# Kernel optimization log

Hardware: AMD Instinct MI355X
Metric: run time of the kernel (lower is better)

Reference implementation:

```python
import jax, jax.numpy as jnp
import numpy as np

GAMMA = 1.0  # gamma=1, train_gamma=False -> constant
K = 3        # kernel_size


def _l2norm(x, axis=-1):
    return x / jnp.sqrt(jnp.sum(x * x, axis=axis, keepdims=True))


def setup_inputs() -> dict:
    key = jax.random.key(0)
    ks = jax.random.split(key, 9)
    B_img, R, D = 48, 36, 1024
    B_cap, T = 48, 32
    Dq = D // 4  # reduce_proj = 4
    s = lambda fan: 1.0 / np.sqrt(fan)
    return {
        "img_embed": jax.random.normal(ks[0], (B_img, R, D), jnp.float32),
        "cap_embed": jax.random.normal(ks[1], (B_cap, T, D), jnp.float32),
        "lens": jax.random.randint(ks[2], (B_cap,), 1, T),
        "Wred": jax.random.normal(ks[3], (Dq, D), jnp.float32) * s(D),
        "bred": jax.random.normal(ks[4], (Dq,), jnp.float32) * s(D),
        "Wproj": jax.random.normal(ks[5], (D * K, Dq), jnp.float32) * s(Dq),
        "bproj": jax.random.normal(ks[6], (D * K,), jnp.float32) * s(Dq),
        "Wconv": jax.random.normal(ks[7], (D, D), jnp.float32) * s(D),
        "bconv": jax.random.normal(ks[8], (D,), jnp.float32) * s(D),
    }


def reference(img_embed, cap_embed, lens, Wred, bred, Wproj, bproj, Wconv, bconv):
    # img_embed: (B, R, D) -> x: (B, D, R);  cap_embed: (Q, T, D)
    B, R, D = img_embed.shape
    Q = cap_embed.shape[0]
    x = jnp.transpose(img_embed, (0, 2, 1))  # (B, D, R)

    # red_txt Conv1d(D, D/4, 1): only token 0 is used downstream
    cap0 = cap_embed[:, 0, :]                                 # (Q, D)
    cap_repr = cap0 @ Wred.T + bred                           # (Q, D/4)

    # dynamic depthwise kernel, softmax-normalized over the K taps
    wdyn = (cap_repr @ Wproj.T + bproj).reshape(Q, D, K)      # (Q, D, K)
    wdyn = jax.nn.softmax(wdyn, axis=-1)

    # depthwise conv (padding=1) applied to the FULL image batch per caption
    xpad = jnp.pad(x, ((0, 0), (0, 0), (1, 1)))
    shifts = jnp.stack([xpad[:, :, h:h + R] for h in range(K)], axis=-1)  # (B,D,R,K)
    conv_dyn = jnp.einsum('bcrk,qck->qbcr', shifts, wdyn)      # (Q, B, D, R)

    # pointwise Conv1d(D, D, 1)
    y = jnp.einsum('qbcr,dc->qbdr', conv_dyn, Wconv) + bconv[None, None, :, None]

    # softmax gate over regions, gated sum-pool, l2norm, cosine sim
    mask = jax.nn.softmax(y * GAMMA, axis=-1)
    img_vec = _l2norm(jnp.sum(mask * y, axis=-1), axis=-1)     # (Q, B, D)
    cap_vec = _l2norm(cap0, axis=-1)                           # (Q, D)
    sims = jnp.einsum('qbd,qd->bq', img_vec, cap_vec)          # (B_img, B_cap)
    return sims
```

## Files before the change

### kernel.cpp

```cpp
#include <hip/hip_runtime.h>

#define D_   1024
#define B_   48
#define Q_   48
#define R_   36
#define RP_  38
#define DQ_  256
#define NPQ_ 1728

typedef __attribute__((ext_vector_type(8))) short bf16x8;
typedef __attribute__((ext_vector_type(8))) unsigned short u16x8;
typedef __attribute__((ext_vector_type(4))) float f32x4;

static __device__ __forceinline__ unsigned short f2bf(float f) {
  union { float f; unsigned u; } v; v.f = f;
  unsigned r = v.u + 0x7fffu + ((v.u >> 16) & 1u);
  return (unsigned short)(r >> 16);
}
static __device__ __forceinline__ float bf2f(unsigned short h) {
  union { unsigned u; float f; } v; v.u = ((unsigned)h) << 16; return v.f;
}
static __device__ __forceinline__ void gload_lds16(const void* g, void* s) {
  __builtin_amdgcn_global_load_lds(
      (const __attribute__((address_space(1))) unsigned int*)g,
      (__attribute__((address_space(3))) unsigned int*)s, 16, 0, 0);
}

__global__ __launch_bounds__(256) void k_capv(const float* __restrict__ cap_embed,
                                              float* __restrict__ capvec)
{
  const int q = blockIdx.x, t = threadIdx.x;
  const int w = t >> 6, lane = t & 63;
  __shared__ float red[4];
  float4 v = ((const float4*)(cap_embed + (size_t)q * 32 * D_))[t];
  float ss = v.x*v.x + v.y*v.y + v.z*v.z + v.w*v.w;
  #pragma unroll
  for (int off = 32; off > 0; off >>= 1) ss += __shfl_down(ss, off);
  if (lane == 0) red[w] = ss;
  __syncthreads();
  float rinv = rsqrtf(red[0] + red[1] + red[2] + red[3]);
  float4 cv; cv.x = v.x*rinv; cv.y = v.y*rinv; cv.z = v.z*rinv; cv.w = v.w*rinv;
  ((float4*)(capvec + (size_t)q * D_))[t] = cv;
}

__global__ __launch_bounds__(256) void k_repr(const float* __restrict__ cap_embed,
    const float* __restrict__ Wred, const float* __restrict__ bred,
    float* __restrict__ repr)
{
  const int q = blockIdx.x;
  const int w = threadIdx.x >> 6, lane = threadIdx.x & 63;
  const int o = blockIdx.y * 4 + w;
  const float4* c4 = (const float4*)(cap_embed + (size_t)q * 32 * D_);
  const float4* wr = (const float4*)(Wred + (size_t)o * D_);
  float acc = 0.f;
  #pragma unroll
  for (int j = 0; j < 4; j++) {
    float4 a = wr[lane + j*64], c = c4[lane + j*64];
    acc += a.x*c.x + a.y*c.y + a.z*c.z + a.w*c.w;
  }
  #pragma unroll
  for (int off = 32; off > 0; off >>= 1) acc += __shfl_down(acc, off);
  if (lane == 0) repr[(size_t)q * DQ_ + o] = acc + bred[o];
}

__global__ __launch_bounds__(256) void k_wdyn(const float* __restrict__ repr,
    const float* __restrict__ Wproj, const float* __restrict__ bproj,
    float* __restrict__ wpl)
{
  const int q = blockIdx.x;
  const int w = threadIdx.x >> 6, lane = threadIdx.x & 63;
  const int d = blockIdx.y * 4 + w;
  float4 r4 = ((const float4*)(repr + (size_t)q * DQ_))[lane];
  float a0, a1, a2;
  {
    const float4* p0 = (const float4*)(Wproj + (size_t)(d*3 + 0) * DQ_);
    const float4* p1 = (const float4*)(Wproj + (size_t)(d*3 + 1) * DQ_);
    const float4* p2 = (const float4*)(Wproj + (size_t)(d*3 + 2) * DQ_);
    float4 v0 = p0[lane], v1 = p1[lane], v2 = p2[lane];
    a0 = v0.x*r4.x + v0.y*r4.y + v0.z*r4.z + v0.w*r4.w;
    a1 = v1.x*r4.x + v1.y*r4.y + v1.z*r4.z + v1.w*r4.w;
    a2 = v2.x*r4.x + v2.y*r4.y + v2.z*r4.z + v2.w*r4.w;
  }
  #pragma unroll
  for (int off = 32; off > 0; off >>= 1) {
    a0 += __shfl_down(a0, off);
    a1 += __shfl_down(a1, off);
    a2 += __shfl_down(a2, off);
  }
  if (lane == 0) {
    float l0 = a0 + bproj[d*3], l1 = a1 + bproj[d*3+1], l2 = a2 + bproj[d*3+2];
    float m = fmaxf(l0, fmaxf(l1, l2));
    float e0 = __expf(l0-m), e1 = __expf(l1-m), e2 = __expf(l2-m);
    float inv = 1.0f / (e0 + e1 + e2);
    wpl[((size_t)q*3 + 0) * D_ + d] = e0 * inv;
    wpl[((size_t)q*3 + 1) * D_ + d] = e1 * inv;
    wpl[((size_t)q*3 + 2) * D_ + d] = e2 * inv;
  }
}

__global__ __launch_bounds__(256) void k_xpad(const float* __restrict__ img,
                                              unsigned short* __restrict__ xpb)
{
  const int br = blockIdx.x;
  const int b = br / RP_, rp = br % RP_;
  const int c = threadIdx.x * 4;
  short4 o;
  if (rp == 0 || rp == RP_ - 1) { o.x = 0; o.y = 0; o.z = 0; o.w = 0; }
  else {
    float4 v = *(const float4*)&img[((size_t)b * R_ + (rp-1)) * D_ + c];
    o.x = (short)f2bf(v.x); o.y = (short)f2bf(v.y);
    o.z = (short)f2bf(v.z); o.w = (short)f2bf(v.w);
  }
  *(short4*)&xpb[(size_t)br * D_ + c] = o;
}

__global__ __launch_bounds__(256) void k_wcbf(const float* __restrict__ Wconv,
                                              unsigned short* __restrict__ wcbf)
{
  const int tid = blockIdx.x * 256 + threadIdx.x;
  const int m = tid >> 7;
  const int gg = tid & 127;
  const int tile = gg >> 2, g = gg & 3;
  const int gl = g ^ ((m >> 1) & 3);
  const float* src = Wconv + (size_t)m * D_ + tile * 32 + gl * 8;
  float4 v0 = *(const float4*)src, v1 = *(const float4*)(src + 4);
  u16x8 o;
  o[0] = f2bf(v0.x); o[1] = f2bf(v0.y); o[2] = f2bf(v0.z); o[3] = f2bf(v0.w);
  o[4] = f2bf(v1.x); o[5] = f2bf(v1.y); o[6] = f2bf(v1.z); o[7] = f2bf(v1.w);
  *(u16x8*)&wcbf[(size_t)m * D_ + tile * 32 + g * 8] = o;
}

__global__ __launch_bounds__(256) void k_cd(const unsigned short* __restrict__ xpb,
    const float* __restrict__ wpl, unsigned short* __restrict__ cd, int qstart)
{
  const int ql = blockIdx.y, qg = qstart + ql;
  const int t = threadIdx.x;
  const int bloc = t >> 7;
  const int b = blockIdx.x * 2 + bloc;
  const int gg = t & 127;
  const int tile = gg >> 2, g = gg & 3;
  const int ch = gg * 8;

  float w0[8], w1[8], w2[8];
  {
    const float4* p0 = (const float4*)(wpl + ((size_t)qg*3 + 0)*D_ + ch);
    const float4* p1 = (const float4*)(wpl + ((size_t)qg*3 + 1)*D_ + ch);
    const float4* p2 = (const float4*)(wpl + ((size_t)qg*3 + 2)*D_ + ch);
    float4 a0 = p0[0], a1 = p0[1], b0 = p1[0], b1 = p1[1], d0 = p2[0], d1 = p2[1];
    w0[0]=a0.x; w0[1]=a0.y; w0[2]=a0.z; w0[3]=a0.w; w0[4]=a1.x; w0[5]=a1.y; w0[6]=a1.z; w0[7]=a1.w;
    w1[0]=b0.x; w1[1]=b0.y; w1[2]=b0.z; w1[3]=b0.w; w1[4]=b1.x; w1[5]=b1.y; w1[6]=b1.z; w1[7]=b1.w;
    w2[0]=d0.x; w2[1]=d0.y; w2[2]=d0.z; w2[3]=d0.w; w2[4]=d1.x; w2[5]=d1.y; w2[6]=d1.z; w2[7]=d1.w;
  }
  const unsigned short* xb = xpb + (size_t)b * RP_ * D_ + ch;
  u16x8 ra = *(const u16x8*)&xb[0];
  u16x8 rb = *(const u16x8*)&xb[D_];
  unsigned short* outb = cd + ((size_t)ql * NPQ_ + (size_t)b * R_) * D_ + tile * 32;
  for (int r = 0; r < R_; r++) {
    u16x8 rc = *(const u16x8*)&xb[(size_t)(r + 2) * D_];
    u16x8 o;
    #pragma unroll
    for (int i = 0; i < 8; i++) {
      float y = w0[i]*bf2f(ra[i]) + w1[i]*bf2f(rb[i]) + w2[i]*bf2f(rc[i]);
      o[i] = f2bf(y);
    }
    int gp = g ^ (((b * 36 + r) >> 1) & 3);
    *(u16x8*)&outb[(size_t)r * D_ + gp * 8] = o;
    ra = rb; rb = rc;
  }
}

#define BM_ 128
#define BN_ 144
#define BK_ 64

__global__ __launch_bounds__(256, 2) void k_gemm(
    const unsigned short* __restrict__ wcbf, const unsigned short* __restrict__ cd,
    const float* __restrict__ bconv, float* __restrict__ imgvec, int qstart)
{
  __shared__ __align__(16) unsigned char smem[37376];
  unsigned short* As = (unsigned short*)smem;
  unsigned short* Bs = (unsigned short*)(smem + 16384);
  float* ep = (float*)smem;

  const int t = threadIdx.x;
  const int w = t >> 6, lane = t & 63;
  const int nt0 = blockIdx.x * BN_;
  const int dt0 = blockIdx.y * BM_;
  const int ql = blockIdx.z, qg = qstart + ql;

  f32x4 acc[2][9];
  #pragma unroll
  for (int mm = 0; mm < 2; mm++)
    #pragma unroll
    for (int nt = 0; nt < 9; nt++)
      acc[mm][nt] = (f32x4){0.f, 0.f, 0.f, 0.f};

  const int lrow = lane >> 2;
  const int lc8  = (lane & 3) * 8;
  const unsigned short* Ag = wcbf + (size_t)dt0 * D_ + lc8;
  const unsigned short* Bg = cd + ((size_t)ql * NPQ_ + nt0) * D_ + lc8;
  const int fr = lane & 15;
  const int fro = fr * 32 + ((((lane >> 4) ^ ((fr >> 1) & 3))) << 3);

  for (int k0 = 0; k0 < D_; k0 += BK_) {
    #pragma unroll
    for (int jj = 0; jj < 2; jj++) {
      int j = w + jj * 4;
      #pragma unroll
      for (int h = 0; h < 2; h++)
        gload_lds16(Ag + (size_t)(j*16 + lrow) * D_ + k0 + h*32,
                    As + (j*2 + h) * 512);
    }
    for (int u = w; u < 18; u += 4) {
      int jb = u >> 1, h = u & 1;
      gload_lds16(Bg + (size_t)(jb*16 + lrow) * D_ + k0 + h*32,
                  Bs + u * 512);
    }
    __syncthreads();
    #pragma unroll
    for (int s = 0; s < 2; s++) {
      bf16x8 aF[2], bF[9];
      #pragma unroll
      for (int mm = 0; mm < 2; mm++)
        aF[mm] = *(const bf16x8*)&As[(w*4 + mm*2 + s) * 512 + fro];
      #pragma unroll
      for (int nt = 0; nt < 9; nt++)
        bF[nt] = *(const bf16x8*)&Bs[(nt*2 + s) * 512 + fro];
      #pragma unroll
      for (int mm = 0; mm < 2; mm++)
        #pragma unroll
        for (int nt = 0; nt < 9; nt++)
          acc[mm][nt] = __builtin_amdgcn_mfma_f32_16x16x32_bf16(aF[mm], bF[nt], acc[mm][nt], 0, 0, 0);
    }
    __syncthreads();
  }

  const int quad = lane >> 4;
  const int b0 = nt0 / R_;
  #pragma unroll
  for (int p = 0; p < 2; p++) {
    #pragma unroll
    for (int mm = 0; mm < 2; mm++)
      #pragma unroll
      for (int nt = 0; nt < 9; nt++) {
        int col = nt * 16 + fr;
        int cl = col - 72 * p;
        if (cl >= 0 && cl < 72) {
          #pragma unroll
          for (int rg = 0; rg < 4; rg++) {
            int row = w * 32 + mm * 16 + quad * 4 + rg;
            ep[row * 73 + cl] = acc[mm][nt][rg];
          }
        }
      }
    __syncthreads();
    {
      int dloc = t >> 1, bloc = t & 1;
      int bg = b0 + p * 2 + bloc;
      const float* yr = ep + dloc * 73 + bloc * 36;
      float m = yr[0];
      for (int r = 1; r < R_; r++) m = fmaxf(m, yr[r]);
      float s = 0.f, wsum = 0.f;
      for (int r = 0; r < R_; r++) {
        float yv = yr[r];
        float e = __expf(yv - m);
        s += e; wsum += e * yv;
      }
      float img = wsum / s + bconv[dt0 + dloc];
      imgvec[((size_t)qg * B_ + bg) * D_ + dt0 + dloc] = img;
    }
    __syncthreads();
  }
}

__global__ __launch_bounds__(256) void k_sims(const float* __restrict__ imgvec,
    const float* __restrict__ capvec, float* __restrict__ out)
{
  const int q = blockIdx.x, b = blockIdx.y, t = threadIdx.x;
  const float4* iv = (const float4*)(imgvec + ((size_t)q * B_ + b) * D_);
  const float4* cv = (const float4*)(capvec + (size_t)q * D_);
  float4 a = iv[t], c = cv[t];
  float ss = a.x*a.x + a.y*a.y + a.z*a.z + a.w*a.w;
  float dt = a.x*c.x + a.y*c.y + a.z*c.z + a.w*c.w;
  #pragma unroll
  for (int off = 32; off > 0; off >>= 1) {
    ss += __shfl_down(ss, off);
    dt += __shfl_down(dt, off);
  }
  __shared__ float r1[4], r2[4];
  if ((t & 63) == 0) { r1[t >> 6] = ss; r2[t >> 6] = dt; }
  __syncthreads();
  if (t == 0) {
    ss = r1[0] + r1[1] + r1[2] + r1[3];
    dt = r2[0] + r2[1] + r2[2] + r2[3];
    out[(size_t)b * Q_ + q] = dt * rsqrtf(ss);
  }
}

extern "C" void kernel_launch(void* const* d_in, const int* in_sizes, int n_in,
                              void* d_out, int out_size, void* d_ws, size_t ws_size,
                              hipStream_t stream)
{
  (void)in_sizes; (void)n_in; (void)out_size;
  const float* img   = (const float*)d_in[0];
  const float* cap   = (const float*)d_in[1];
  const float* Wred  = (const float*)d_in[3];
  const float* bred  = (const float*)d_in[4];
  const float* Wproj = (const float*)d_in[5];
  const float* bproj = (const float*)d_in[6];
  const float* Wconv = (const float*)d_in[7];
  const float* bconv = (const float*)d_in[8];
  float* out = (float*)d_out;

  char* ws = (char*)d_ws;
  const size_t XPB_B  = (size_t)B_ * RP_ * D_ * 2;
  const size_t WCBF_B = (size_t)D_ * D_ * 2;
  const size_t WPL_B  = (size_t)Q_ * 3 * D_ * 4;
  const size_t CAPV_B = (size_t)Q_ * D_ * 4;
  const size_t REPR_B = (size_t)Q_ * DQ_ * 4;
  const size_t IMGV_B = (size_t)Q_ * B_ * D_ * 4;
  unsigned short* xpb  = (unsigned short*)ws;
  unsigned short* wcbf = (unsigned short*)(ws + XPB_B);
  float* wpl    = (float*)(ws + XPB_B + WCBF_B);
  float* capvec = (float*)(ws + XPB_B + WCBF_B + WPL_B);
  float* repr   = (float*)(ws + XPB_B + WCBF_B + WPL_B + CAPV_B);
  float* imgvec = (float*)(ws + XPB_B + WCBF_B + WPL_B + CAPV_B + REPR_B);
  const size_t FIXED = XPB_B + WCBF_B + WPL_B + CAPV_B + REPR_B + IMGV_B;
  unsigned short* cdbuf = (unsigned short*)(ws + FIXED);
  const size_t PERQ = (size_t)NPQ_ * D_ * 2;

  int qchunk = 1;
  if (ws_size > FIXED + PERQ) {
    size_t c = (ws_size - FIXED) / PERQ;
    qchunk = (c > (size_t)Q_) ? Q_ : (int)c;
  }

  k_capv<<<dim3(Q_), dim3(256), 0, stream>>>(cap, capvec);
  k_repr<<<dim3(Q_, 64), dim3(256), 0, stream>>>(cap, Wred, bred, repr);
  k_wdyn<<<dim3(Q_, 256), dim3(256), 0, stream>>>(repr, Wproj, bproj, wpl);
  k_xpad<<<dim3(B_ * RP_), dim3(256), 0, stream>>>(img, xpb);
  k_wcbf<<<dim3(512), dim3(256), 0, stream>>>(Wconv, wcbf);
  for (int q0 = 0; q0 < Q_; q0 += qchunk) {
    int qs = (Q_ - q0 < qchunk) ? (Q_ - q0) : qchunk;
    k_cd<<<dim3(B_ / 2, qs), dim3(256), 0, stream>>>(xpb, wpl, cdbuf, q0);
    k_gemm<<<dim3(NPQ_ / BN_, D_ / BM_, qs), dim3(256), 0, stream>>>(wcbf, cdbuf, bconv, imgvec, q0);
  }
  k_sims<<<dim3(Q_, B_), dim3(256), 0, stream>>>(imgvec, capvec, out);
}
```

Baseline: 323.8 us.

## Double GEMM M-tile to 256 rows and fold caption norm into sims kernel

The pointwise-conv GEMM tile grows from 128 to 256 output channels per block. Each wave now holds 4x9 MFMA accumulators, which raises reuse of the B (conv output) tile and halves B-tile global traffic. The epilogue is split into two 128-row passes so the shared-memory staging buffer still fits. The separate caption-normalisation kernel is removed and its norm is computed inside the sims kernel, saving one launch. The cost is roughly double the accumulator registers (144 floats), which risks losing occupancy under launch_bounds(256,2), plus larger LDS use and half as many blocks in the grid.

```diff
diff --git a/kernel.cpp b/kernel.cpp
--- a/kernel.cpp
+++ b/kernel.cpp
@@ -24,23 +24,6 @@
   __builtin_amdgcn_global_load_lds(
       (const __attribute__((address_space(1))) unsigned int*)g,
       (__attribute__((address_space(3))) unsigned int*)s, 16, 0, 0);
-}
-
-__global__ __launch_bounds__(256) void k_capv(const float* __restrict__ cap_embed,
-                                              float* __restrict__ capvec)
-{
-  const int q = blockIdx.x, t = threadIdx.x;
-  const int w = t >> 6, lane = t & 63;
-  __shared__ float red[4];
-  float4 v = ((const float4*)(cap_embed + (size_t)q * 32 * D_))[t];
-  float ss = v.x*v.x + v.y*v.y + v.z*v.z + v.w*v.w;
-  #pragma unroll
-  for (int off = 32; off > 0; off >>= 1) ss += __shfl_down(ss, off);
-  if (lane == 0) red[w] = ss;
-  __syncthreads();
-  float rinv = rsqrtf(red[0] + red[1] + red[2] + red[3]);
-  float4 cv; cv.x = v.x*rinv; cv.y = v.y*rinv; cv.z = v.z*rinv; cv.w = v.w*rinv;
-  ((float4*)(capvec + (size_t)q * D_))[t] = cv;
 }
 
 __global__ __launch_bounds__(256) void k_repr(const float* __restrict__ cap_embed,
@@ -169,7 +152,7 @@
   }
 }
 
-#define BM_ 128
+#define BM_ 256
 #define BN_ 144
 #define BK_ 64
 
@@ -177,9 +160,9 @@
     const unsigned short* __restrict__ wcbf, const unsigned short* __restrict__ cd,
     const float* __restrict__ bconv, float* __restrict__ imgvec, int qstart)
 {
-  __shared__ __align__(16) unsigned char smem[37376];
+  __shared__ __align__(16) unsigned char smem[51200];
   unsigned short* As = (unsigned short*)smem;
-  unsigned short* Bs = (unsigned short*)(smem + 16384);
+  unsigned short* Bs = (unsigned short*)(smem + 32768);
   float* ep = (float*)smem;
 
   const int t = threadIdx.x;
@@ -188,9 +171,9 @@
   const int dt0 = blockIdx.y * BM_;
   const int ql = blockIdx.z, qg = qstart + ql;
 
-  f32x4 acc[2][9];
-  #pragma unroll
-  for (int mm = 0; mm < 2; mm++)
+  f32x4 acc[4][9];
+  #pragma unroll
+  for (int mm = 0; mm < 4; mm++)
     #pragma unroll
     for (int nt = 0; nt < 9; nt++)
       acc[mm][nt] = (f32x4){0.f, 0.f, 0.f, 0.f};
@@ -204,30 +187,27 @@
 
   for (int k0 = 0; k0 < D_; k0 += BK_) {
     #pragma unroll
-    for (int jj = 0; jj < 2; jj++) {
-      int j = w + jj * 4;
-      #pragma unroll
-      for (int h = 0; h < 2; h++)
-        gload_lds16(Ag + (size_t)(j*16 + lrow) * D_ + k0 + h*32,
-                    As + (j*2 + h) * 512);
+    for (int jj = 0; jj < 8; jj++) {
+      int u = w + jj * 4;
+      int ja = u >> 1, h = u & 1;
+      gload_lds16(Ag + (size_t)(ja*16 + lrow) * D_ + k0 + h*32, As + u * 512);
     }
     for (int u = w; u < 18; u += 4) {
       int jb = u >> 1, h = u & 1;
-      gload_lds16(Bg + (size_t)(jb*16 + lrow) * D_ + k0 + h*32,
-                  Bs + u * 512);
+      gload_lds16(Bg + (size_t)(jb*16 + lrow) * D_ + k0 + h*32, Bs + u * 512);
     }
     __syncthreads();
     #pragma unroll
     for (int s = 0; s < 2; s++) {
-      bf16x8 aF[2], bF[9];
+      bf16x8 aF[4], bF[9];
       #pragma unroll
-      for (int mm = 0; mm < 2; mm++)
-        aF[mm] = *(const bf16x8*)&As[(w*4 + mm*2 + s) * 512 + fro];
+      for (int mm = 0; mm < 4; mm++)
+        aF[mm] = *(const bf16x8*)&As[((w*4 + mm)*2 + s) * 512 + fro];
       #pragma unroll
       for (int nt = 0; nt < 9; nt++)
         bF[nt] = *(const bf16x8*)&Bs[(nt*2 + s) * 512 + fro];
       #pragma unroll
-      for (int mm = 0; mm < 2; mm++)
+      for (int mm = 0; mm < 4; mm++)
         #pragma unroll
         for (int nt = 0; nt < 9; nt++)
           acc[mm][nt] = __builtin_amdgcn_mfma_f32_16x16x32_bf16(aF[mm], bF[nt], acc[mm][nt], 0, 0, 0);
@@ -238,62 +218,71 @@
   const int quad = lane >> 4;
   const int b0 = nt0 / R_;
   #pragma unroll
-  for (int p = 0; p < 2; p++) {
-    #pragma unroll
-    for (int mm = 0; mm < 2; mm++)
-      #pragma unroll
-      for (int nt = 0; nt < 9; nt++) {
-        int col = nt * 16 + fr;
-        int cl = col - 72 * p;
-        if (cl >= 0 && cl < 72) {
+  for (int pp = 0; pp < 2; pp++) {
+    #pragma unroll
+    for (int p = 0; p < 2; p++) {
+      if ((w >> 1) == pp) {
+        #pragma unroll
+        for (int mm = 0; mm < 4; mm++)
           #pragma unroll
-          for (int rg = 0; rg < 4; rg++) {
-            int row = w * 32 + mm * 16 + quad * 4 + rg;
-            ep[row * 73 + cl] = acc[mm][nt][rg];
+          for (int nt = 0; nt < 9; nt++) {
+            int col = nt * 16 + fr;
+            int cl = col - 72 * p;
+            if (cl >= 0 && cl < 72) {
+              #pragma unroll
+              for (int rg = 0; rg < 4; rg++) {
+                int rloc = (w & 1) * 64 + mm * 16 + quad * 4 + rg;
+                ep[rloc * 73 + cl] = acc[mm][nt][rg];
+              }
+            }
           }
+      }
+      __syncthreads();
+      {
+        int dloc = t >> 1, bloc = t & 1;
+        int bg = b0 + p * 2 + bloc;
+        int dg = dt0 + pp * 128 + dloc;
+        const float* yr = ep + dloc * 73 + bloc * 36;
+        float m = yr[0];
+        for (int r = 1; r < R_; r++) m = fmaxf(m, yr[r]);
+        float s = 0.f, wsum = 0.f;
+        for (int r = 0; r < R_; r++) {
+          float yv = yr[r];
+          float e = __expf(yv - m);
+          s += e; wsum += e * yv;
         }
+        float img = wsum / s + bconv[dg];
+        imgvec[((size_t)qg * B_ + bg) * D_ + dg] = img;
       }
-    __syncthreads();
-    {
-      int dloc = t >> 1, bloc = t & 1;
-      int bg = b0 + p * 2 + bloc;
-      const float* yr = ep + dloc * 73 + bloc * 36;
-      float m = yr[0];
-      for (int r = 1; r < R_; r++) m = fmaxf(m, yr[r]);
-      float s = 0.f, wsum = 0.f;
-      for (int r = 0; r < R_; r++) {
-        float yv = yr[r];
-        float e = __expf(yv - m);
-        s += e; wsum += e * yv;
-      }
-      float img = wsum / s + bconv[dt0 + dloc];
-      imgvec[((size_t)qg * B_ + bg) * D_ + dt0 + dloc] = img;
-    }
-    __syncthreads();
+      __syncthreads();
+    }
   }
 }
 
 __global__ __launch_bounds__(256) void k_sims(const float* __restrict__ imgvec,
-    const float* __restrict__ capvec, float* __restrict__ out)
+    const float* __restrict__ cap_embed, float* __restrict__ out)
 {
   const int q = blockIdx.x, b = blockIdx.y, t = threadIdx.x;
   const float4* iv = (const float4*)(imgvec + ((size_t)q * B_ + b) * D_);
-  const float4* cv = (const float4*)(capvec + (size_t)q * D_);
+  const float4* cv = (const float4*)(cap_embed + (size_t)q * 32 * D_);
   float4 a = iv[t], c = cv[t];
   float ss = a.x*a.x + a.y*a.y + a.z*a.z + a.w*a.w;
+  float sc = c.x*c.x + c.y*c.y + c.z*c.z + c.w*c.w;
   float dt = a.x*c.x + a.y*c.y + a.z*c.z + a.w*c.w;
   #pragma unroll
   for (int off = 32; off > 0; off >>= 1) {
     ss += __shfl_down(ss, off);
+    sc += __shfl_down(sc, off);
     dt += __shfl_down(dt, off);
   }
-  __shared__ float r1[4], r2[4];
-  if ((t & 63) == 0) { r1[t >> 6] = ss; r2[t >> 6] = dt; }
+  __shared__ float r1[4], r2[4], r3[4];
+  if ((t & 63) == 0) { r1[t >> 6] = ss; r2[t >> 6] = sc; r3[t >> 6] = dt; }
   __syncthreads();
   if (t == 0) {
     ss = r1[0] + r1[1] + r1[2] + r1[3];
-    dt = r2[0] + r2[1] + r2[2] + r2[3];
-    out[(size_t)b * Q_ + q] = dt * rsqrtf(ss);
+    sc = r2[0] + r2[1] + r2[2] + r2[3];
+    dt = r3[0] + r3[1] + r3[2] + r3[3];
+    out[(size_t)b * Q_ + q] = dt * rsqrtf(ss) * rsqrtf(sc);
   }
 }
 
@@ -316,16 +305,14 @@
   const size_t XPB_B  = (size_t)B_ * RP_ * D_ * 2;
   const size_t WCBF_B = (size_t)D_ * D_ * 2;
   const size_t WPL_B  = (size_t)Q_ * 3 * D_ * 4;
-  const size_t CAPV_B = (size_t)Q_ * D_ * 4;
   const size_t REPR_B = (size_t)Q_ * DQ_ * 4;
   const size_t IMGV_B = (size_t)Q_ * B_ * D_ * 4;
   unsigned short* xpb  = (unsigned short*)ws;
   unsigned short* wcbf = (unsigned short*)(ws + XPB_B);
   float* wpl    = (float*)(ws + XPB_B + WCBF_B);
-  float* capvec = (float*)(ws + XPB_B + WCBF_B + WPL_B);
-  float* repr   = (float*)(ws + XPB_B + WCBF_B + WPL_B + CAPV_B);
-  float* imgvec = (float*)(ws + XPB_B + WCBF_B + WPL_B + CAPV_B + REPR_B);
-  const size_t FIXED = XPB_B + WCBF_B + WPL_B + CAPV_B + REPR_B + IMGV_B;
+  float* repr   = (float*)(ws + XPB_B + WCBF_B + WPL_B);
+  float* imgvec = (float*)(ws + XPB_B + WCBF_B + WPL_B + REPR_B);
+  const size_t FIXED = XPB_B + WCBF_B + WPL_B + REPR_B + IMGV_B;
   unsigned short* cdbuf = (unsigned short*)(ws + FIXED);
   const size_t PERQ = (size_t)NPQ_ * D_ * 2;
 
@@ -335,7 +322,6 @@
     qchunk = (c > (size_t)Q_) ? Q_ : (int)c;
   }
 
-  k_capv<<<dim3(Q_), dim3(256), 0, stream>>>(cap, capvec);
   k_repr<<<dim3(Q_, 64), dim3(256), 0, stream>>>(cap, Wred, bred, repr);
   k_wdyn<<<dim3(Q_, 256), dim3(256), 0, stream>>>(repr, Wproj, bproj, wpl);
   k_xpad<<<dim3(B_ * RP_), dim3(256), 0, stream>>>(img, xpb);
@@ -345,5 +331,5 @@
     k_cd<<<dim3(B_ / 2, qs), dim3(256), 0, stream>>>(xpb, wpl, cdbuf, q0);
     k_gemm<<<dim3(NPQ_ / BN_, D_ / BM_, qs), dim3(256), 0, stream>>>(wcbf, cdbuf, bconv, imgvec, q0);
   }
-  k_sims<<<dim3(Q_, B_), dim3(256), 0, stream>>>(imgvec, capvec, out);
-}
+  k_sims<<<dim3(Q_, B_), dim3(256), 0, stream>>>(imgvec, cap, out);
+}
```

After: 289.0 us. -10.7%, faster.
